# Optimization experiments

Hardware: AMD Instinct MI355X
Metric: run time of the kernel (lower is better)

Reference implementation:

```python
import jax, jax.numpy as jnp
import numpy as np

EMB = 64
N_LEFT = 100000   # m: rows of left_features, b
N_RIGHT = 100000  # n: rows of right_features, c
N_EDGES = 3200000


def setup_inputs() -> dict:
    key = jax.random.key(0)
    ks = jax.random.split(key, 12)
    inp = {
        "left_features": jax.random.normal(ks[0], (N_LEFT, EMB), jnp.float32),
        "right_features_k": jax.random.normal(ks[1], (N_RIGHT, EMB), jnp.float32),
        "edge_index": jax.random.randint(ks[2], (N_EDGES, 2), 0, N_RIGHT, jnp.int64),
        "edge_weight": jax.random.uniform(ks[3], (N_EDGES,), jnp.float32),
        "right_features": jax.random.normal(ks[4], (N_RIGHT, EMB), jnp.float32),
        "c": jax.random.normal(ks[5], (N_RIGHT, 1), jnp.float32),
        "b": jax.random.normal(ks[6], (N_LEFT, 1), jnp.float32),
        # learned parameters
        "temp": jnp.full((2,), 0.9, jnp.float32),
        "W1": jax.random.normal(ks[7], (EMB, EMB), jnp.float32) * 0.05,
        "b1": jnp.zeros((EMB,), jnp.float32),
        "W2": jax.random.normal(ks[8], (EMB, EMB), jnp.float32) * 0.05,
        "b2": jnp.zeros((EMB,), jnp.float32),
    }
    return inp


def reference(left_features, right_features_k, edge_index, edge_weight,
              right_features, c, b, temp, W1, b1, W2, b2):
    # right_to_left=False branch of BipartiteGraphConvolution.forward
    n = right_features.shape[0]  # = c.shape[0]
    # Source quirk: values.sum(dim=-1) on a 1-D vector is a GLOBAL scalar sum,
    # clamped to min 1; every edge weight is scaled by 1/that scalar.
    total = jnp.maximum(jnp.sum(edge_weight), 1.0)
    vals = edge_weight / total                                    # [E]
    row = edge_index[:, 0]  # destination (right) node, in [0, n)
    col = edge_index[:, 1]  # source (left) node, in [0, m)
    # sparse-dense matmul: conv_output = A @ left_features, A in COO (coalesce
    # just sums duplicate entries, identical to segment-sum over raw edges)
    msg = left_features[col] * vals[:, None]                      # [E, EMB]
    conv_output = jax.ops.segment_sum(msg, row, num_segments=n)   # [n, EMB]
    h = right_features + temp[1] * (c - conv_output)              # [n, EMB]
    # output_module: Linear -> ReLU -> Linear (torch Linear: x @ W.T + b)
    h = jax.nn.relu(h @ W1.T + b1)
    out = h @ W2.T + b2
    return out
```

## Files before the change

kernel.cpp:

```cpp
#include <hip/hip_runtime.h>

#define EMB 64
#define BROWS 512
#define BSHIFT 9
#define CHUNK 4096
#define COLBITS 23
#define COLMASK ((1u << COLBITS) - 1u)
#define MROWS 64
#define HPAD 66

__device__ __forceinline__ unsigned short f2bf(float f) {
    unsigned u = __float_as_uint(f);
    u = u + 0x7FFFu + ((u >> 16) & 1u);
    return (unsigned short)(u >> 16);
}

__global__ void convert_left_kernel(const float* __restrict__ left,
                                    unsigned* __restrict__ left16, int n2) {
    int i = blockIdx.x * blockDim.x + threadIdx.x;
    if (i >= n2) return;
    float2 v = ((const float2*)left)[i];
    left16[i] = (unsigned)f2bf(v.x) | ((unsigned)f2bf(v.y) << 16);
}

__global__ void init_bcur_kernel(int* __restrict__ bcur, int nb, int slot) {
    int t = threadIdx.x;
    if (t < nb) bcur[t] = t * slot;
}

__global__ __launch_bounds__(256) void partition_kernel(
    const int2* __restrict__ eidx, const float* __restrict__ w, int n_edges,
    int* __restrict__ bcursor, int2* __restrict__ bsorted,
    float* __restrict__ total) {
    __shared__ int lcur[256];
    __shared__ int lo[256];
    __shared__ int go[256];
    __shared__ int ps[256];
    __shared__ int2 stage[CHUNK];
    __shared__ int dstg[CHUNK];
    int t = threadIdx.x;
    int base = blockIdx.x * CHUNK;
    int cnt = min(CHUNK, n_edges - base);

    lcur[t] = 0;
    __syncthreads();

    int2 pay[CHUNK / 256];
    int meta[CHUNK / 256];
    float s = 0.f;
    #pragma unroll
    for (int k = 0; k < CHUNK / 256; ++k) {
        int e = base + t + k * 256;
        if (e < n_edges) {
            int2 rc = eidx[e];
            float wv = w[e];
            s += wv;
            int b = rc.x >> BSHIFT;
            unsigned rl = (unsigned)(rc.x & (BROWS - 1));
            pay[k] = make_int2((int)((rl << COLBITS) | (unsigned)rc.y),
                               __float_as_int(wv));
            int rank = atomicAdd(&lcur[b], 1);
            meta[k] = (b << 16) | rank;
        } else {
            meta[k] = -1;
        }
    }
    #pragma unroll
    for (int off = 32; off > 0; off >>= 1) s += __shfl_down(s, off, 64);
    if ((t & 63) == 0) atomicAdd(total, s);
    __syncthreads();

    int v = lcur[t];
    ps[t] = v;
    __syncthreads();
    for (int off = 1; off < 256; off <<= 1) {
        int u = (t >= off) ? ps[t - off] : 0;
        __syncthreads();
        ps[t] += u;
        __syncthreads();
    }
    lo[t] = ps[t] - v;
    go[t] = (v > 0) ? atomicAdd(&bcursor[t], v) : 0;
    __syncthreads();

    #pragma unroll
    for (int k = 0; k < CHUNK / 256; ++k) {
        int m = meta[k];
        if (m >= 0) {
            int b = m >> 16;
            int rank = m & 0xffff;
            int p = lo[b] + rank;
            stage[p] = pay[k];
            dstg[p] = go[b] + rank;
        }
    }
    __syncthreads();

    #pragma unroll
    for (int k = 0; k < CHUNK / 256; ++k) {
        int s2 = t + k * 256;
        if (s2 < cnt) bsorted[dstg[s2]] = stage[s2];
    }
}

__global__ __launch_bounds__(256, 1) void count_scan_kernel(
    const int* __restrict__ bcur, int* __restrict__ sbase, int nb, int slot) {
    __shared__ int ssc[256];
    int t = threadIdx.x;
    int cnt = (t < nb) ? (bcur[t] - t * slot) : 0;
    ssc[t] = cnt;
    __syncthreads();
    for (int off = 1; off < 256; off <<= 1) {
        int u = (t >= off) ? ssc[t - off] : 0;
        __syncthreads();
        ssc[t] += u;
        __syncthreads();
    }
    if (t < nb) sbase[t] = ssc[t] - cnt;
}

__global__ __launch_bounds__(1024) void local_rowsort_kernel(
    const int2* __restrict__ bsorted, const int* __restrict__ bcur,
    const int* __restrict__ sbase, int* __restrict__ offs,
    int2* __restrict__ sorted2, int n_right, int slot) {
    __shared__ int lhist[BROWS];
    __shared__ int lcur[BROWS];
    __shared__ int ps[BROWS];
    int b = blockIdx.x;
    int t = threadIdx.x;
    int src0 = b * slot;
    int send = min(bcur[b], src0 + slot);
    int dbase = sbase[b];
    int row0 = b << BSHIFT;
    int nrows = min(BROWS, n_right - row0);

    if (t < BROWS) lhist[t] = 0;
    __syncthreads();
    for (int e = src0 + t; e < send; e += 1024)
        atomicAdd(&lhist[((unsigned)bsorted[e].x) >> COLBITS], 1);
    __syncthreads();

    if (t < BROWS) ps[t] = lhist[t];
    __syncthreads();
    for (int off = 1; off < BROWS; off <<= 1) {
        int u = (t < BROWS && t >= off) ? ps[t - off] : 0;
        __syncthreads();
        if (t < BROWS) ps[t] += u;
        __syncthreads();
    }
    if (t < BROWS) {
        int excl = ps[t] - lhist[t];
        lcur[t] = excl;
        if (t < nrows) offs[row0 + t] = dbase + excl;
    }
    __syncthreads();

    int e = src0 + t;
    for (; e + 3 * 1024 < send; e += 4 * 1024) {
        int2 e0 = bsorted[e + 0 * 1024];
        int2 e1 = bsorted[e + 1 * 1024];
        int2 e2 = bsorted[e + 2 * 1024];
        int2 e3 = bsorted[e + 3 * 1024];
        int p0 = atomicAdd(&lcur[((unsigned)e0.x) >> COLBITS], 1);
        int p1 = atomicAdd(&lcur[((unsigned)e1.x) >> COLBITS], 1);
        int p2 = atomicAdd(&lcur[((unsigned)e2.x) >> COLBITS], 1);
        int p3 = atomicAdd(&lcur[((unsigned)e3.x) >> COLBITS], 1);
        sorted2[dbase + p0] = e0;
        sorted2[dbase + p1] = e1;
        sorted2[dbase + p2] = e2;
        sorted2[dbase + p3] = e3;
    }
    for (; e < send; e += 1024) {
        int2 e0 = bsorted[e];
        int p0 = atomicAdd(&lcur[((unsigned)e0.x) >> COLBITS], 1);
        sorted2[dbase + p0] = e0;
    }
}

__global__ void seg_gather_bf16_kernel(const int2* __restrict__ sorted,
                                       const int* __restrict__ offs,
                                       const uint4* __restrict__ left16o,
                                       const float* __restrict__ right,
                                       const float* __restrict__ c,
                                       const float* __restrict__ temp,
                                       const float* __restrict__ total,
                                       float* __restrict__ hout, int n_right,
                                       int n_edges, int offs_are_ends) {
    int gid = blockIdx.x * blockDim.x + threadIdx.x;
    int wid = gid >> 6;
    int lane = gid & 63;
    if (wid >= n_right) return;
    int start, end;
    if (offs_are_ends) {
        end = offs[wid];
        start = (wid == 0) ? 0 : offs[wid - 1];
    } else {
        start = offs[wid];
        end = (wid + 1 < n_right) ? offs[wid + 1] : n_edges;
    }

    int sub = lane >> 3;
    int d8  = lane & 7;

    float cv = c[wid];
    float inv = 1.0f / fmaxf(total[0], 1.0f);
    float t1 = temp[1];

    float a0 = 0.f, a1 = 0.f, a2 = 0.f, a3 = 0.f;
    float a4 = 0.f, a5 = 0.f, a6 = 0.f, a7 = 0.f;

    if (start < end) {
        int last = end - 1;
        int i0 = start + sub;
        int2 s0 = sorted[min(i0, last)];
        int2 s1 = sorted[min(i0 + 8, last)];
        for (int base = start; base < end; base += 16) {
            int2 c0 = s0;
            int2 c1 = s1;
            int nb0 = base + 16;
            if (nb0 < end) {
                s0 = sorted[min(nb0 + sub, last)];
                s1 = sorted[min(nb0 + 8 + sub, last)];
            }
            float w0 = (base + sub < end) ? __int_as_float(c0.y) : 0.f;
            float w1 = (base + 8 + sub < end) ? __int_as_float(c1.y) : 0.f;
            unsigned col0 = (unsigned)c0.x & COLMASK;
            unsigned col1 = (unsigned)c1.x & COLMASK;
            uint4 p0 = left16o[(size_t)col0 * 8 + d8];
            uint4 p1 = left16o[(size_t)col1 * 8 + d8];
            a0 = fmaf(w0, __uint_as_float(p0.x << 16), a0);
            a1 = fmaf(w0, __uint_as_float(p0.x & 0xffff0000u), a1);
            a2 = fmaf(w0, __uint_as_float(p0.y << 16), a2);
            a3 = fmaf(w0, __uint_as_float(p0.y & 0xffff0000u), a3);
            a4 = fmaf(w0, __uint_as_float(p0.z << 16), a4);
            a5 = fmaf(w0, __uint_as_float(p0.z & 0xffff0000u), a5);
            a6 = fmaf(w0, __uint_as_float(p0.w << 16), a6);
            a7 = fmaf(w0, __uint_as_float(p0.w & 0xffff0000u), a7);
            a0 = fmaf(w1, __uint_as_float(p1.x << 16), a0);
            a1 = fmaf(w1, __uint_as_float(p1.x & 0xffff0000u), a1);
            a2 = fmaf(w1, __uint_as_float(p1.y << 16), a2);
            a3 = fmaf(w1, __uint_as_float(p1.y & 0xffff0000u), a3);
            a4 = fmaf(w1, __uint_as_float(p1.z << 16), a4);
            a5 = fmaf(w1, __uint_as_float(p1.z & 0xffff0000u), a5);
            a6 = fmaf(w1, __uint_as_float(p1.w << 16), a6);
            a7 = fmaf(w1, __uint_as_float(p1.w & 0xffff0000u), a7);
        }
    }

    #define RED8(x) x += __shfl_xor(x, 8, 64); x += __shfl_xor(x, 16, 64); \
                    x += __shfl_xor(x, 32, 64);
    RED8(a0) RED8(a1) RED8(a2) RED8(a3) RED8(a4) RED8(a5) RED8(a6) RED8(a7)
    #undef RED8

    if (lane < 8) {
        const float4* rp = (const float4*)(right + (size_t)wid * EMB);
        float4 r0 = rp[2 * lane];
        float4 r1 = rp[2 * lane + 1];
        float4 h0, h1;
        h0.x = r0.x + t1 * (cv - a0 * inv);
        h0.y = r0.y + t1 * (cv - a1 * inv);
        h0.z = r0.z + t1 * (cv - a2 * inv);
        h0.w = r0.w + t1 * (cv - a3 * inv);
        h1.x = r1.x + t1 * (cv - a4 * inv);
        h1.y = r1.y + t1 * (cv - a5 * inv);
        h1.z = r1.z + t1 * (cv - a6 * inv);
        h1.w = r1.w + t1 * (cv - a7 * inv);
        float4* op = (float4*)(hout + (size_t)wid * EMB);
        op[2 * lane] = h0;
        op[2 * lane + 1] = h1;
    }
}

__global__ __launch_bounds__(256, 4) void mlp_kernel(
    const float* __restrict__ W1, const float* __restrict__ b1,
    const float* __restrict__ W2, const float* __restrict__ b2,
    float* __restrict__ io, int n) {
    __shared__ float hT[64 * HPAD];
    __shared__ float h1T[64 * 64];
    int t = threadIdx.x;
    int r = t & 63;
    int q = __builtin_amdgcn_readfirstlane(t >> 6);
    int row0 = blockIdx.x * MROWS;

    #pragma unroll
    for (int i = 0; i < 16; ++i) {
        int rr = i * 4 + q;
        int gr = row0 + rr;
        float v = (gr < n) ? io[(size_t)gr * EMB + r] : 0.f;
        hT[r * HPAD + rr] = v;
    }
    __syncthreads();

    float acc[16];
    #pragma unroll
    for (int jj = 0; jj < 16; ++jj) acc[jj] = b1[q * 16 + jj];
    for (int k = 0; k < 64; ++k) {
        float hk = hT[k * HPAD + r];
        #pragma unroll
        for (int jj = 0; jj < 16; ++jj)
            acc[jj] = fmaf(hk, W1[(q * 16 + jj) * EMB + k], acc[jj]);
    }
    #pragma unroll
    for (int jj = 0; jj < 16; ++jj)
        h1T[(q * 16 + jj) * 64 + r] = fmaxf(acc[jj], 0.f);
    __syncthreads();

    #pragma unroll
    for (int jj = 0; jj < 16; ++jj) acc[jj] = b2[q * 16 + jj];
    for (int k = 0; k < 64; ++k) {
        float hk = h1T[k * 64 + r];
        #pragma unroll
        for (int jj = 0; jj < 16; ++jj)
            acc[jj] = fmaf(hk, W2[(q * 16 + jj) * EMB + k], acc[jj]);
    }
    __syncthreads();
    #pragma unroll
    for (int jj = 0; jj < 16; ++jj)
        hT[(q * 16 + jj) * HPAD + r] = acc[jj];
    __syncthreads();

    #pragma unroll
    for (int i = 0; i < 16; ++i) {
        int rr = i * 4 + q;
        int gr = row0 + rr;
        if (gr < n) io[(size_t)gr * EMB + r] = hT[r * HPAD + rr];
    }
}


__global__ void hist_total_kernel(const int2* __restrict__ eidx,
                                  const float* __restrict__ w, int n_edges,
                                  int* __restrict__ counts,
                                  float* __restrict__ total) {
    int gid = blockIdx.x * blockDim.x + threadIdx.x;
    int stride = gridDim.x * blockDim.x;
    float s = 0.f;
    for (int e = gid; e < n_edges; e += stride) {
        s += w[e];
        atomicAdd(&counts[eidx[e].x], 1);
    }
    #pragma unroll
    for (int off = 32; off > 0; off >>= 1) s += __shfl_down(s, off, 64);
    if ((threadIdx.x & 63) == 0) atomicAdd(total, s);
}

__global__ __launch_bounds__(1024, 1) void scan1_kernel(
    const int* __restrict__ cnt, int* __restrict__ incl,
    int* __restrict__ bsums, int n) {
    __shared__ int s[1024];
    int t = threadIdx.x;
    int i = blockIdx.x * 1024 + t;
    int v = (i < n) ? cnt[i] : 0;
    s[t] = v;
    __syncthreads();
    for (int off = 1; off < 1024; off <<= 1) {
        int u = (t >= off) ? s[t - off] : 0;
        __syncthreads();
        s[t] += u;
        __syncthreads();
    }
    if (i < n) incl[i] = s[t];
    if (t == 1023) bsums[blockIdx.x] = s[t];
}

__global__ __launch_bounds__(256, 1) void scan2_kernel(int* __restrict__ bsums, int nb) {
    __shared__ int s[256];
    int t = threadIdx.x;
    int v = (t < nb) ? bsums[t] : 0;
    s[t] = v;
    __syncthreads();
    for (int off = 1; off < 256; off <<= 1) {
        int u = (t >= off) ? s[t - off] : 0;
        __syncthreads();
        s[t] += u;
        __syncthreads();
    }
    if (t < nb) bsums[t] = s[t] - v;
}

__global__ void scan3_kernel(const int* __restrict__ incl,
                             const int* __restrict__ base,
                             int* __restrict__ offs, int n) {
    int i = blockIdx.x * blockDim.x + threadIdx.x;
    if (i >= n) return;
    offs[i] = (i == 0) ? 0 : incl[i - 1] + base[(i - 1) >> 10];
}

__global__ void scatter_kernel(const int2* __restrict__ eidx,
                               const float* __restrict__ w, int n_edges,
                               int* __restrict__ offs,
                               int2* __restrict__ sorted) {
    int gid = blockIdx.x * blockDim.x + threadIdx.x;
    int stride = gridDim.x * blockDim.x;
    for (int e = gid; e < n_edges; e += stride) {
        int2 rc = eidx[e];
        float v = w[e];
        int pos = atomicAdd(&offs[rc.x], 1);
        sorted[pos] = make_int2(rc.y, __float_as_int(v));
    }
}


__global__ void sum_weights_kernel(const float* __restrict__ w, int n,
                                   float* __restrict__ total) {
    int gid = blockIdx.x * blockDim.x + threadIdx.x;
    int stride = gridDim.x * blockDim.x;
    float s = 0.f;
    for (int i = gid; i < n; i += stride) s += w[i];
    #pragma unroll
    for (int off = 32; off > 0; off >>= 1) s += __shfl_down(s, off, 64);
    if ((threadIdx.x & 63) == 0) atomicAdd(total, s);
}

__global__ void edge_scatter_kernel(const int* __restrict__ idx,
                                    const float* __restrict__ w,
                                    const float* __restrict__ left,
                                    const float* __restrict__ total,
                                    float* __restrict__ conv,
                                    long long n_threads) {
    long long gid = (long long)blockIdx.x * blockDim.x + threadIdx.x;
    if (gid >= n_threads) return;
    int e = (int)(gid >> 6);
    int d = (int)(gid & 63);
    float inv = 1.0f / fmaxf(total[0], 1.0f);
    int row = idx[2 * e];
    int col = idx[2 * e + 1];
    float v = w[e] * inv;
    float msg = left[(size_t)col * EMB + d] * v;
    atomicAdd(&conv[(size_t)row * EMB + d], msg);
}

__global__ __launch_bounds__(256, 1) void fused_mlp_kernel(
    const float* __restrict__ right, const float* __restrict__ c,
    const float* __restrict__ temp,
    const float* __restrict__ W1, const float* __restrict__ b1,
    const float* __restrict__ W2, const float* __restrict__ b2,
    float* __restrict__ io, int n) {
    int r = blockIdx.x * blockDim.x + threadIdx.x;
    if (r >= n) return;
    float t1 = temp[1];
    float cv = c[r];
    float h[EMB];
    const float4* rp = (const float4*)(right + (size_t)r * EMB);
    const float4* qp = (const float4*)(io + (size_t)r * EMB);
    #pragma unroll
    for (int qq = 0; qq < EMB / 4; ++qq) {
        float4 rv = rp[qq];
        float4 qv = qp[qq];
        h[4 * qq + 0] = rv.x + t1 * (cv - qv.x);
        h[4 * qq + 1] = rv.y + t1 * (cv - qv.y);
        h[4 * qq + 2] = rv.z + t1 * (cv - qv.z);
        h[4 * qq + 3] = rv.w + t1 * (cv - qv.w);
    }
    float h1[EMB];
    #pragma unroll
    for (int j = 0; j < EMB; j += 4) {
        float s0 = b1[j], s1 = b1[j + 1], s2 = b1[j + 2], s3 = b1[j + 3];
        #pragma unroll
        for (int k = 0; k < EMB; ++k) {
            float hk = h[k];
            s0 = fmaf(hk, W1[(j + 0) * EMB + k], s0);
            s1 = fmaf(hk, W1[(j + 1) * EMB + k], s1);
            s2 = fmaf(hk, W1[(j + 2) * EMB + k], s2);
            s3 = fmaf(hk, W1[(j + 3) * EMB + k], s3);
        }
        h1[j] = fmaxf(s0, 0.f);
        h1[j + 1] = fmaxf(s1, 0.f);
        h1[j + 2] = fmaxf(s2, 0.f);
        h1[j + 3] = fmaxf(s3, 0.f);
    }
    float4* op = (float4*)(io + (size_t)r * EMB);
    #pragma unroll
    for (int j = 0; j < EMB; j += 4) {
        float s0 = b2[j], s1 = b2[j + 1], s2 = b2[j + 2], s3 = b2[j + 3];
        #pragma unroll
        for (int k = 0; k < EMB; ++k) {
            float hk = h1[k];
            s0 = fmaf(hk, W2[(j + 0) * EMB + k], s0);
            s1 = fmaf(hk, W2[(j + 1) * EMB + k], s1);
            s2 = fmaf(hk, W2[(j + 2) * EMB + k], s2);
            s3 = fmaf(hk, W2[(j + 3) * EMB + k], s3);
        }
        op[j / 4] = make_float4(s0, s1, s2, s3);
    }
}


extern "C" void kernel_launch(void* const* d_in, const int* in_sizes, int n_in,
                              void* d_out, int out_size, void* d_ws, size_t ws_size,
                              hipStream_t stream) {
    const float* left   = (const float*)d_in[0];
    const int*   eidx   = (const int*)d_in[2];
    const float* ew     = (const float*)d_in[3];
    const float* right  = (const float*)d_in[4];
    const float* c      = (const float*)d_in[5];
    const float* temp   = (const float*)d_in[7];
    const float* W1     = (const float*)d_in[8];
    const float* b1     = (const float*)d_in[9];
    const float* W2     = (const float*)d_in[10];
    const float* b2     = (const float*)d_in[11];

    const int n_edges = in_sizes[3];
    const int n_right = in_sizes[4] / EMB;
    const int n_left  = in_sizes[0] / EMB;
    float* out = (float*)d_out;

    const int nb = (n_right + BROWS - 1) >> BSHIFT;
    const int nblocks_scan = (n_right + 1023) / 1024;

    auto align256 = [](size_t x) { return (x + 255) & ~(size_t)255; };

    int slot = n_edges / (nb > 0 ? nb : 1);
    slot += slot / 16 + 128;

    size_t off_bcur    = 64;
    size_t off_sbase   = align256(off_bcur + (size_t)nb * 4);
    size_t off_offs    = align256(off_sbase + (size_t)(nb + 1) * 4);
    size_t off_bsorted = align256(off_offs + (size_t)n_right * 4);
    size_t off_sorted2 = align256(off_bsorted + ((size_t)nb * slot + slot) * 8);
    size_t off_left16f = align256(off_sorted2 + (size_t)n_edges * 8);
    size_t req_full    = off_left16f + (size_t)n_left * EMB * 2;

    size_t m_off_offs   = 64;
    size_t m_off_incl   = align256(m_off_offs + (size_t)n_right * 4);
    size_t m_off_bsum   = align256(m_off_incl + (size_t)n_right * 4);
    size_t m_off_sorted = align256(m_off_bsum + 1024);
    size_t m_off_left16 = align256(m_off_sorted + (size_t)n_edges * 8);
    size_t req_mid      = m_off_left16 + (size_t)n_left * EMB * 2;

    bool common_ok = (nb <= 256) && (nblocks_scan <= 256) &&
                     (n_left <= (1 << COLBITS)) && (BROWS * nb >= n_right) &&
                     (CHUNK <= 65536);

    if (common_ok && ws_size >= req_full) {
        char* ws = (char*)d_ws;
        float* total = (float*)ws;
        int* bcur = (int*)(ws + off_bcur);
        int* sbase = (int*)(ws + off_sbase);
        int* offs = (int*)(ws + off_offs);
        int2* bsorted = (int2*)(ws + off_bsorted);
        int2* sorted2 = (int2*)(ws + off_sorted2);
        unsigned short* left16 = (unsigned short*)(ws + off_left16f);

        hipMemsetAsync(ws, 0, 64, stream);

        int n2 = n_left * EMB / 2;
        convert_left_kernel<<<(n2 + 255) / 256, 256, 0, stream>>>(
            left, (unsigned*)left16, n2);
        init_bcur_kernel<<<1, 256, 0, stream>>>(bcur, nb, slot);
        {
            int nchunks = (n_edges + CHUNK - 1) / CHUNK;
            partition_kernel<<<nchunks, 256, 0, stream>>>(
                (const int2*)eidx, ew, n_edges, bcur, bsorted, total);
        }
        count_scan_kernel<<<1, 256, 0, stream>>>(bcur, sbase, nb, slot);
        local_rowsort_kernel<<<nb, 1024, 0, stream>>>(bsorted, bcur, sbase, offs,
                                                      sorted2, n_right, slot);
        {
            long long n_threads = (long long)n_right * EMB;
            int blocks = (int)((n_threads + 255) / 256);
            seg_gather_bf16_kernel<<<blocks, 256, 0, stream>>>(
                sorted2, offs, (const uint4*)left16, right, c, temp, total,
                out, n_right, n_edges, 0);
        }
        mlp_kernel<<<(n_right + MROWS - 1) / MROWS, 256, 0, stream>>>(
            W1, b1, W2, b2, out, n_right);
    } else if (common_ok && ws_size >= req_mid) {
        char* ws = (char*)d_ws;
        float* total = (float*)ws;
        int* offs = (int*)(ws + m_off_offs);
        int* incl = (int*)(ws + m_off_incl);
        int* bsum = (int*)(ws + m_off_bsum);
        int2* sorted = (int2*)(ws + m_off_sorted);
        unsigned short* left16 = (unsigned short*)(ws + m_off_left16);

        hipMemsetAsync(ws, 0, m_off_offs + (size_t)n_right * 4, stream);

        int n2 = n_left * EMB / 2;
        convert_left_kernel<<<(n2 + 255) / 256, 256, 0, stream>>>(
            left, (unsigned*)left16, n2);
        hist_total_kernel<<<2048, 256, 0, stream>>>((const int2*)eidx, ew,
                                                    n_edges, offs, total);
        scan1_kernel<<<nblocks_scan, 1024, 0, stream>>>(offs, incl, bsum, n_right);
        scan2_kernel<<<1, 256, 0, stream>>>(bsum, nblocks_scan);
        scan3_kernel<<<(n_right + 255) / 256, 256, 0, stream>>>(incl, bsum, offs,
                                                                n_right);
        scatter_kernel<<<2048, 256, 0, stream>>>((const int2*)eidx, ew, n_edges,
                                                 offs, sorted);
        {
            long long n_threads = (long long)n_right * EMB;
            int blocks = (int)((n_threads + 255) / 256);
            seg_gather_bf16_kernel<<<blocks, 256, 0, stream>>>(
                sorted, offs, (const uint4*)left16, right, c, temp, total,
                out, n_right, n_edges, 1);
        }
        mlp_kernel<<<(n_right + MROWS - 1) / MROWS, 256, 0, stream>>>(
            W1, b1, W2, b2, out, n_right);
    } else {
        float* total = (float*)d_ws;
        hipMemsetAsync(d_out, 0, (size_t)out_size * sizeof(float), stream);
        hipMemsetAsync(d_ws, 0, sizeof(float), stream);
        sum_weights_kernel<<<2048, 256, 0, stream>>>(ew, n_edges, total);
        long long n_threads = (long long)n_edges * EMB;
        long long blocks = (n_threads + 255) / 256;
        edge_scatter_kernel<<<(int)blocks, 256, 0, stream>>>(
            eidx, ew, left, total, out, n_threads);
        int mblocks = (n_right + 255) / 256;
        fused_mlp_kernel<<<mblocks, 256, 0, stream>>>(right, c, temp, W1, b1, W2,
                                                      b2, out, n_right);
    }
}
```

Measured before the change: 227.1 us.

## Fuse histogram and scatter in local rowsort by caching edges and ranks in registers

The local row sort now loads each bucket's edges once into registers and takes a per-row rank via a shared atomic during that load. The same counts feed the prefix scan, and the final scatter uses the cached payloads plus offset and rank. This removes a second global read of the bucket and one round of shared-memory atomics. In exchange it raises register use and adds a guard that falls back to the other path when a bucket slot exceeds KMAX*1024 edges.

```diff
diff --git a/kernel.cpp b/kernel.cpp
--- a/kernel.cpp
+++ b/kernel.cpp
@@ -8,6 +8,7 @@
 #define COLMASK ((1u << COLBITS) - 1u)
 #define MROWS 64
 #define HPAD 66
+#define KMAX 20
 
 __device__ __forceinline__ unsigned short f2bf(float f) {
     unsigned u = __float_as_uint(f);
@@ -123,7 +124,6 @@
     const int2* __restrict__ bsorted, const int* __restrict__ bcur,
     const int* __restrict__ sbase, int* __restrict__ offs,
     int2* __restrict__ sorted2, int n_right, int slot) {
-    __shared__ int lhist[BROWS];
     __shared__ int lcur[BROWS];
     __shared__ int ps[BROWS];
     int b = blockIdx.x;
@@ -134,13 +134,28 @@
     int row0 = b << BSHIFT;
     int nrows = min(BROWS, n_right - row0);
 
-    if (t < BROWS) lhist[t] = 0;
-    __syncthreads();
-    for (int e = src0 + t; e < send; e += 1024)
-        atomicAdd(&lhist[((unsigned)bsorted[e].x) >> COLBITS], 1);
-    __syncthreads();
-
-    if (t < BROWS) ps[t] = lhist[t];
+    if (t < BROWS) lcur[t] = 0;
+    __syncthreads();
+
+    int2 pay[KMAX];
+    int meta[KMAX];
+    #pragma unroll
+    for (int k = 0; k < KMAX; ++k) {
+        int e = src0 + t + k * 1024;
+        if (e < send) {
+            int2 v = bsorted[e];
+            pay[k] = v;
+            unsigned row = ((unsigned)v.x) >> COLBITS;
+            int rank = atomicAdd(&lcur[row], 1);
+            meta[k] = (int)((row << 18) | (unsigned)rank);
+        } else {
+            meta[k] = -1;
+        }
+    }
+    __syncthreads();
+
+    int v = (t < BROWS) ? lcur[t] : 0;
+    if (t < BROWS) ps[t] = v;
     __syncthreads();
     for (int off = 1; off < BROWS; off <<= 1) {
         int u = (t < BROWS && t >= off) ? ps[t - off] : 0;
@@ -149,31 +164,20 @@
         __syncthreads();
     }
     if (t < BROWS) {
-        int excl = ps[t] - lhist[t];
+        int excl = ps[t] - v;
         lcur[t] = excl;
         if (t < nrows) offs[row0 + t] = dbase + excl;
     }
     __syncthreads();
 
-    int e = src0 + t;
-    for (; e + 3 * 1024 < send; e += 4 * 1024) {
-        int2 e0 = bsorted[e + 0 * 1024];
-        int2 e1 = bsorted[e + 1 * 1024];
-        int2 e2 = bsorted[e + 2 * 1024];
-        int2 e3 = bsorted[e + 3 * 1024];
-        int p0 = atomicAdd(&lcur[((unsigned)e0.x) >> COLBITS], 1);
-        int p1 = atomicAdd(&lcur[((unsigned)e1.x) >> COLBITS], 1);
-        int p2 = atomicAdd(&lcur[((unsigned)e2.x) >> COLBITS], 1);
-        int p3 = atomicAdd(&lcur[((unsigned)e3.x) >> COLBITS], 1);
-        sorted2[dbase + p0] = e0;
-        sorted2[dbase + p1] = e1;
-        sorted2[dbase + p2] = e2;
-        sorted2[dbase + p3] = e3;
-    }
-    for (; e < send; e += 1024) {
-        int2 e0 = bsorted[e];
-        int p0 = atomicAdd(&lcur[((unsigned)e0.x) >> COLBITS], 1);
-        sorted2[dbase + p0] = e0;
+    #pragma unroll
+    for (int k = 0; k < KMAX; ++k) {
+        int m = meta[k];
+        if (m >= 0) {
+            int row = ((unsigned)m) >> 18;
+            int rank = m & ((1 << 18) - 1);
+            sorted2[dbase + lcur[row] + rank] = pay[k];
+        }
     }
 }
 
@@ -529,10 +533,10 @@
     size_t req_mid      = m_off_left16 + (size_t)n_left * EMB * 2;
 
     bool common_ok = (nb <= 256) && (nblocks_scan <= 256) &&
-                     (n_left <= (1 << COLBITS)) && (BROWS * nb >= n_right) &&
-                     (CHUNK <= 65536);
-
-    if (common_ok && ws_size >= req_full) {
+                     (n_left <= (1 << COLBITS)) && (BROWS * nb >= n_right);
+    bool full_ok = common_ok && (slot <= KMAX * 1024) && (slot < (1 << 18));
+
+    if (full_ok && ws_size >= req_full) {
         char* ws = (char*)d_ws;
         float* total = (float*)ws;
         int* bcur = (int*)(ws + off_bcur);
```

Measured after the change: 228.3 us. About the same (+0.5%).
